# Optimization experiments

Hardware: AMD Instinct MI355X
Metric: run time of the kernel (lower is better)

The kernel has to match this reference:

```python
import jax, jax.numpy as jnp
import numpy as np

T, B, N_IN, H, N_OUT = 32, 32, 64, 256, 64
CLAMP_MIN, CLAMP_MAX = -2.0, 2.0  # scalar `min`/`max` forward args of the torch module


def setup_inputs() -> dict:
    key = jax.random.key(0)
    ks = jax.random.split(key, 8)
    s_ih = 1.0 / np.sqrt(N_IN)
    s_hh = 1.0 / np.sqrt(H)
    X = jax.random.normal(ks[0], (T, B, N_IN), jnp.float32)
    eps = jax.random.uniform(ks[1], (B,), jnp.float32) * 0.1  # per-sample perturbation radius
    W_ih = jax.random.normal(ks[2], (N_IN, H), jnp.float32) * s_ih  # already transposed, as in forward
    W_hh = jax.random.normal(ks[3], (H, H), jnp.float32) * s_hh
    b_ih = jax.random.normal(ks[4], (H,), jnp.float32) * s_hh
    b_hh = jax.random.normal(ks[5], (H,), jnp.float32) * s_hh
    W_o = jax.random.normal(ks[6], (H, N_OUT), jnp.float32) * s_hh
    b_o = jax.random.normal(ks[7], (N_OUT,), jnp.float32) * s_hh
    return dict(X=X, eps=eps, W_ih=W_ih, W_hh=W_hh, b_ih=b_ih, b_hh=b_hh, W_o=W_o, b_o=b_o)


def _zono_tanh(head, err):
    # DeepZ-style abstract tanh transformer on a zonotope (head [B,H], err [B,E,H]).
    rad = jnp.sum(jnp.abs(err), axis=1)                  # [B,H] concretization radius
    l, u = head - rad, head + rad
    tl, tu = jnp.tanh(l), jnp.tanh(u)
    lam = jnp.minimum(1.0 - tl * tl, 1.0 - tu * tu)      # minimal slope on [l,u]
    mu = 0.5 * (tu + tl - lam * (u + l))
    delta = 0.5 * (tu - tl - lam * (u - l))              # new error magnitude (>=0)
    new_head = lam * head + mu
    new_err = jnp.concatenate([lam[:, None, :] * err,
                               jax.vmap(jnp.diag)(delta)], axis=1)  # append H fresh symbols
    return new_head, new_err


def reference(X, eps, W_ih, W_hh, b_ih, b_hh, W_o, b_o):
    Bsz, Hn = X.shape[1], W_hh.shape[0]
    head_h = jnp.zeros((Bsz, Hn), X.dtype)
    err_h = jnp.zeros((Bsz, 0, Hn), X.dtype)
    bias = b_ih + b_hh
    for t in range(X.shape[0]):  # sequential recurrence; T is static
        x = X[t]                                          # [B, N_IN]
        l = jnp.maximum(x - eps[:, None], CLAMP_MIN)      # clamp(x-eps, min=min)
        u = jnp.minimum(x + eps[:, None], CLAMP_MAX)      # clamp(x+eps, max=max)
        head_x = 0.5 * (l + u)
        err_x = jax.vmap(jnp.diag)(0.5 * (u - l))         # diag_embed -> [B, N_IN, N_IN]
        # affine zonotope step: hx + hi + b_ih + b_hh
        head = head_x @ W_ih + head_h @ W_hh + bias       # [B, H]
        err = jnp.concatenate([err_h @ W_hh, err_x @ W_ih], axis=1)  # [B, E+N_IN, H]
        head_h, err_h = _zono_tanh(head, err)
    # output layer on the final zonotope; return concretized [lower, upper] bounds
    head_out = head_h @ W_o + b_o                         # [B, N_OUT]
    rad_out = jnp.sum(jnp.abs(err_h @ W_o), axis=1)       # [B, N_OUT]
    return jnp.stack([head_out - rad_out, head_out + rad_out])  # [2, B, N_OUT]
```

## Files before the change

### kernel.cpp

```cpp
#include <hip/hip_runtime.h>
#include <math.h>

typedef unsigned short u16;
typedef unsigned long long u64;
typedef __attribute__((ext_vector_type(8))) short bf16x8;
typedef __attribute__((ext_vector_type(4))) float f32x4;

#define T_STEPS 32
#define BSZ     32
#define N_IN    64
#define H       256
#define N_OUT   64
#define ESTRIDE 9984
#define CLAMP_MIN (-2.0f)
#define CLAMP_MAX ( 2.0f)
#define GNB 16


__device__ inline u16 f2bf(float x) {
    unsigned u = __builtin_bit_cast(unsigned, x);
    unsigned r = u + 0x7FFFu + ((u >> 16) & 1u);
    return (u16)(r >> 16);
}
__device__ inline float bf2f(short s) {
    return __builtin_bit_cast(float, ((unsigned)(u16)s) << 16);
}

__device__ __forceinline__ void gl_lds16(const u16* g, u16* l) {
    __builtin_amdgcn_global_load_lds(
        (const __attribute__((address_space(1))) unsigned int*)g,
        (__attribute__((address_space(3))) unsigned int*)l,
        16, 0, 0);
}

__global__ void transpose_k(const float* __restrict__ src, float* __restrict__ dst,
                            int R, int C)
{
    __shared__ float tile[32][33];
    int bi = blockIdx.y, bj = blockIdx.x;
    int r0 = threadIdx.x >> 5, c = threadIdx.x & 31;
    #pragma unroll
    for (int rr = 0; rr < 4; ++rr) {
        int r = r0 * 4 + rr;
        tile[r][c] = src[(bi * 32 + r) * C + bj * 32 + c];
    }
    __syncthreads();
    #pragma unroll
    for (int rr = 0; rr < 4; ++rr) {
        int r = r0 * 4 + rr;
        dst[(bj * 32 + r) * R + bi * 32 + c] = tile[c][r];
    }
}

__global__ void packPairs_k(const float* __restrict__ W, float* __restrict__ WP)
{
    int p = blockIdx.x * 256 + threadIdx.x;
    int vb = (p & 1) * 2, hh = (p >> 1) & 1, m = (p >> 2) & 15, qq = (p >> 6) & 3;
    int KC = (p >> 8) & 7, RT = p >> 11;
    int i = RT * 16 + m, k = KC * 32 + qq * 8 + hh * 4 + vb;
    ((float2*)WP)[p] = make_float2(W[(size_t)i * H + k], W[(size_t)i * H + k + 1]);
}

__global__ void packWT_k(const float* __restrict__ WT32, u16* __restrict__ WTp)
{
    int p = blockIdx.x * 256 + threadIdx.x;
    int vb = (p & 1) * 2, hh = (p >> 1) & 1, m = (p >> 2) & 15, qq = (p >> 6) & 3;
    int KC = (p >> 8) & 7, RT = p >> 11;
    int n = RT * 16 + m, k = KC * 32 + qq * 8 + hh * 4 + vb;
    *(unsigned*)&WTp[2 * p] =
          (unsigned)f2bf(WT32[(size_t)n * H + k])
        | ((unsigned)f2bf(WT32[(size_t)n * H + k + 1]) << 16);
}

__global__ __launch_bounds__(256) void prefresh_k(
    const float* __restrict__ X, const float* __restrict__ eps,
    const float* __restrict__ Wih, const float* __restrict__ WihP,
    const float* __restrict__ bih, const float* __restrict__ bhh,
    u16* __restrict__ err, float* __restrict__ radT, float* __restrict__ hp0)
{
    __shared__ float rho_s[N_IN], hx_s[N_IN];
    const int t = blockIdx.x, bi = blockIdx.y, tid = threadIdx.x;
    if (tid < N_IN) {
        float x = X[((size_t)t * BSZ + bi) * N_IN + tid], e = eps[bi];
        float lo = fmaxf(x - e, CLAMP_MIN), up = fminf(x + e, CLAMP_MAX);
        rho_s[tid] = 0.5f * (up - lo);
        hx_s[tid]  = 0.5f * (up + lo);
    }
    __syncthreads();

    float s = 0.f;
    #pragma unroll 8
    for (int i = 0; i < N_IN; ++i)
        s += fabsf(rho_s[i]) * fabsf(Wih[(size_t)i * H + tid]);
    radT[(size_t)t * BSZ * H + (size_t)bi * H + tid] = s;

    if (t == 0) {
        float acc = bih[tid] + bhh[tid];
        #pragma unroll 8
        for (int i = 0; i < N_IN; ++i) acc += hx_s[i] * Wih[i * H + tid];
        hp0[bi * H + tid] = acc;
    }

    u16* dst = err + (size_t)bi * ESTRIDE * H + (size_t)(20 * t) * 4096;
    const float2* wp = (const float2*)WihP;
    #pragma unroll 4
    for (int iter = 0; iter < 32; ++iter) {
        int p = iter * 256 + tid;
        int i = (p >> 11) * 16 + ((p >> 2) & 15);
        float2 w = wp[p];
        float rho = rho_s[i];
        *(unsigned*)&dst[2 * p] =
            (unsigned)f2bf(rho * w.x) | ((unsigned)f2bf(rho * w.y) << 16);
    }
}

__global__ __launch_bounds__(256, 2) void step_k(
    const float* __restrict__ Xt, const float* __restrict__ eps,
    const float* __restrict__ Wih, const float* __restrict__ Whh,
    const float* __restrict__ WhhP, const u16* __restrict__ WhhTp,
    const float* __restrict__ bih, const float* __restrict__ bhh,
    const float* __restrict__ hp_prev, const float* __restrict__ rad_prev,
    float* __restrict__ hp_new, float* __restrict__ rad_new,
    u16* __restrict__ err, int E_old)
{
    __shared__ u16 sbuf[4][8192];
    __shared__ float lam_s[H], de_s[H], hh_s[H], hx_s[N_IN];
    const int bx = blockIdx.x, b = blockIdx.y, tid = threadIdx.x;
    const int ntiles = (E_old - H) >> 5;
    u16* errB = err + (size_t)b * ESTRIDE * H;
    const int wave = tid >> 6, lane = tid & 63;
    const int m = lane & 15, q = lane >> 4;
    const bool gem = (bx < ntiles);

    if (gem) {
        #pragma unroll
        for (int j = 0; j < 3; ++j) {
            int tj = bx + j * GNB;
            if (tj < ntiles) {
                const u16* g = errB + (size_t)tj * 8192;
                #pragma unroll
                for (int r = 0; r < 4; ++r)
                    gl_lds16(g + r * 2048 + tid * 8, &sbuf[j][r * 2048 + wave * 512]);
            }
        }
    }

    bf16x8 bf[4][8];
    if (gem) {
        #pragma unroll
        for (int nt = 0; nt < 4; ++nt)
            #pragma unroll
            for (int kc = 0; kc < 8; ++kc)
                bf[nt][kc] = *(const bf16x8*)
                    &WhhTp[(size_t)(((((wave * 4 + nt) * 8 + kc) * 4 + q) << 7) + m * 8)];
    }

    {
        float hd = hp_prev[b * H + tid], rv = rad_prev[b * H + tid];
        float lo = hd - rv, up = hd + rv;
        float tl = tanhf(lo), tu = tanhf(up);
        float la = fminf(1.f - tl * tl, 1.f - tu * tu);
        float mu = 0.5f * (tu + tl - la * (up + lo));
        float dd = 0.5f * (tu - tl - la * (up - lo));
        lam_s[tid] = la;
        de_s[tid]  = dd;
        hh_s[tid]  = la * hd + mu;
    }
    asm volatile("s_waitcnt lgkmcnt(0)" ::: "memory");
    __builtin_amdgcn_s_barrier();

    if (gem) {
        #pragma unroll
        for (int nt = 0; nt < 4; ++nt)
            #pragma unroll
            for (int kc = 0; kc < 8; ++kc) {
                const int k0 = kc * 32 + q * 8;
                float4 la = *(const float4*)&lam_s[k0];
                float4 lb = *(const float4*)&lam_s[k0 + 4];
                bf16x8 w = bf[nt][kc], f;
                f[0] = (short)f2bf(bf2f(w[0]) * la.x);
                f[1] = (short)f2bf(bf2f(w[1]) * la.y);
                f[2] = (short)f2bf(bf2f(w[2]) * la.z);
                f[3] = (short)f2bf(bf2f(w[3]) * la.w);
                f[4] = (short)f2bf(bf2f(w[4]) * lb.x);
                f[5] = (short)f2bf(bf2f(w[5]) * lb.y);
                f[6] = (short)f2bf(bf2f(w[6]) * lb.z);
                f[7] = (short)f2bf(bf2f(w[7]) * lb.w);
                bf[nt][kc] = f;
            }

        float racc[16];
        #pragma unroll
        for (int i = 0; i < 16; ++i) racc[i] = 0.f;

        asm volatile("s_waitcnt vmcnt(0)" ::: "memory");
        __builtin_amdgcn_s_barrier();

        int cur = 0;
        for (int tile = bx; tile < ntiles; tile += GNB) {
            int pf = tile + 3 * GNB;
            if (pf < ntiles) {
                const u16* g = errB + (size_t)pf * 8192;
                #pragma unroll
                for (int r = 0; r < 4; ++r)
                    gl_lds16(g + r * 2048 + tid * 8,
                             &sbuf[(cur + 3) & 3][r * 2048 + wave * 512]);
            }

            f32x4 acc[2][4];
            #pragma unroll
            for (int i = 0; i < 2; ++i)
                #pragma unroll
                for (int c = 0; c < 4; ++c) acc[i][c] = (f32x4){0.f, 0.f, 0.f, 0.f};

            #pragma unroll
            for (int kc = 0; kc < 8; ++kc) {
                bf16x8 af[2];
                #pragma unroll
                for (int rt = 0; rt < 2; ++rt)
                    af[rt] = *(const bf16x8*)
                        &sbuf[cur][(((rt * 8 + kc) * 4 + q) << 7) + m * 8];
                #pragma unroll
                for (int nt = 0; nt < 4; ++nt)
                    #pragma unroll
                    for (int rt = 0; rt < 2; ++rt)
                        acc[rt][nt] = __builtin_amdgcn_mfma_f32_16x16x32_bf16(
                            bf[nt][kc], af[rt], acc[rt][nt], 0, 0, 0);
            }

            #pragma unroll
            for (int rt = 0; rt < 2; ++rt) {
                const size_t rowbase = (size_t)(tile * 2 + rt) * 4096;
                #pragma unroll
                for (int nt = 0; nt < 4; ++nt) {
                    f32x4 v = acc[rt][nt];
                    racc[nt * 4 + 0] += fabsf(v[0]);
                    racc[nt * 4 + 1] += fabsf(v[1]);
                    racc[nt * 4 + 2] += fabsf(v[2]);
                    racc[nt * 4 + 3] += fabsf(v[3]);
                    unsigned lo = (unsigned)f2bf(v[0]) | ((unsigned)f2bf(v[1]) << 16);
                    unsigned hi = (unsigned)f2bf(v[2]) | ((unsigned)f2bf(v[3]) << 16);
                    const int NT  = wave * 4 + nt;
                    const int kcs = NT >> 1;
                    const int qq  = (NT & 1) * 2 + (q >> 1);
                    const size_t off16 = rowbase
                        + (size_t)(((kcs * 4 + qq) << 7) + m * 8 + (q & 1) * 4);
                    *(u64*)&errB[off16] = ((u64)hi << 32) | lo;
                }
            }
            asm volatile("s_waitcnt vmcnt(32)" ::: "memory");
            __builtin_amdgcn_s_barrier();
            cur = (cur + 1) & 3;
        }

        #pragma unroll
        for (int i = 0; i < 16; ++i) {
            float v = racc[i];
            v += __shfl_xor(v, 1);
            v += __shfl_xor(v, 2);
            v += __shfl_xor(v, 4);
            v += __shfl_xor(v, 8);
            if (m == 0) {
                int nt = i >> 2, vv = i & 3;
                atomicAdd(&rad_new[b * H + wave * 64 + nt * 16 + q * 4 + vv], v);
            }
        }
    }

    const int diagRTbase = (E_old - H) >> 4;
    const float2* wp = (const float2*)WhhP;
    u16* dbase = errB + (size_t)(diagRTbase + bx) * 4096;
    #pragma unroll
    for (int iter = 0; iter < 8; ++iter) {
        int p = iter * 256 + tid;
        int mm = (p >> 2) & 15;
        float dv = de_s[bx * 16 + mm];
        float2 w = wp[bx * 2048 + p];
        *(unsigned*)&dbase[2 * p] =
            (unsigned)f2bf(dv * w.x) | ((unsigned)f2bf(dv * w.y) << 16);
    }
    float s = 0.f;
    #pragma unroll
    for (int ii = 0; ii < 16; ++ii) {
        int i = bx * 16 + ii;
        s += fabsf(de_s[i]) * fabsf(Whh[(size_t)i * H + tid]);
    }
    atomicAdd(&rad_new[b * H + tid], s);

    if (bx == GNB - 1) {
        if (tid < N_IN) {
            float x = Xt[b * N_IN + tid], e = eps[b];
            float l2 = fmaxf(x - e, CLAMP_MIN), u2 = fminf(x + e, CLAMP_MAX);
            hx_s[tid] = 0.5f * (l2 + u2);
        }
        __syncthreads();
        float acc = bih[tid] + bhh[tid];
        #pragma unroll 8
        for (int i = 0; i < N_IN; ++i) acc += hx_s[i] * Wih[i * H + tid];
        #pragma unroll 8
        for (int j = 0; j < H; ++j) acc += hh_s[j] * Whh[j * H + tid];
        hp_new[b * H + tid] = acc;
    }
}

__global__ __launch_bounds__(256) void tanh_final_k(
    const float* __restrict__ hp, const float* __restrict__ rad,
    float* __restrict__ lam, float* __restrict__ de, float* __restrict__ head_h)
{
    const int b = blockIdx.x, h = threadIdx.x;
    float hd = hp[b * H + h], r = rad[b * H + h];
    float l = hd - r, u = hd + r;
    float tl = tanhf(l), tu = tanhf(u);
    float la = fminf(1.f - tl * tl, 1.f - tu * tu);
    float mu = 0.5f * (tu + tl - la * (u + l));
    float dd = 0.5f * (tu - tl - la * (u - l));
    lam[b * H + h] = la;
    de[b * H + h]  = dd;
    head_h[b * H + h] = la * hd + mu;
}

__global__ __launch_bounds__(256) void packWoT_k(
    const float* __restrict__ WoT32, const float* __restrict__ lam,
    u16* __restrict__ WoTp)
{
    const int b = blockIdx.x, tid = threadIdx.x;
    __shared__ float lam_s[H];
    lam_s[tid] = lam[b * H + tid];
    __syncthreads();
    u16* dst = WoTp + (size_t)b * N_OUT * H;
    #pragma unroll 4
    for (int iter = 0; iter < 32; ++iter) {
        int p = iter * 256 + tid;
        int vb = (p & 1) * 2, hh = (p >> 1) & 1, m = (p >> 2) & 15, qq = (p >> 6) & 3;
        int KC = (p >> 8) & 7, RT = p >> 11;
        int n = RT * 16 + m, k = KC * 32 + qq * 8 + hh * 4 + vb;
        *(unsigned*)&dst[2 * p] =
              (unsigned)f2bf(lam_s[k]     * WoT32[(size_t)n * H + k])
            | ((unsigned)f2bf(lam_s[k + 1] * WoT32[(size_t)n * H + k + 1]) << 16);
    }
}

__global__ void head_out_k(
    const float* __restrict__ head_h, const float* __restrict__ de,
    const float* __restrict__ Wo, const float* __restrict__ bo,
    float* __restrict__ head_out, float* __restrict__ rad_out)
{
    const int b = blockIdx.x, o = threadIdx.x;
    float acc = bo[o], accR = 0.f;
    #pragma unroll 4
    for (int j = 0; j < H; ++j) {
        float w = Wo[j * N_OUT + o];
        acc  += head_h[b * H + j] * w;
        accR += fabsf(de[b * H + j] * w);
    }
    head_out[b * N_OUT + o] = acc;
    rad_out[b * N_OUT + o]  = accR;
}

__global__ __launch_bounds__(256) void gemm_out_k(
    const u16* __restrict__ err, const u16* __restrict__ WoTp,
    float* __restrict__ rad_out)
{
    __shared__ float rad_s[N_OUT];
    const int b = blockIdx.y, row0 = blockIdx.x * 256, tid = threadIdx.x;
    const int wave = tid >> 6, lane = tid & 63;
    const int m = lane & 15, q = lane >> 4;
    const u16* errB = err + (size_t)b * ESTRIDE * H;
    const u16* Wb   = WoTp + (size_t)b * N_OUT * H;

    if (tid < N_OUT) rad_s[tid] = 0.f;
    __syncthreads();

    f32x4 acc[4][4];
    #pragma unroll
    for (int i = 0; i < 4; ++i)
        #pragma unroll
        for (int c = 0; c < 4; ++c) acc[i][c] = (f32x4){0.f, 0.f, 0.f, 0.f};

    const int tile0 = (row0 >> 4) + wave * 4;
    #pragma unroll
    for (int kc = 0; kc < 8; ++kc) {
        bf16x8 af[4], bw[4];
        #pragma unroll
        for (int rt = 0; rt < 4; ++rt)
            af[rt] = *(const bf16x8*)
                &errB[(size_t)(((((tile0 + rt) * 8 + kc) * 4 + q) << 7) + m * 8)];
        #pragma unroll
        for (int nt = 0; nt < 4; ++nt)
            bw[nt] = *(const bf16x8*)
                &Wb[(size_t)((((nt * 8 + kc) * 4 + q) << 7) + m * 8)];
        #pragma unroll
        for (int nt = 0; nt < 4; ++nt)
            #pragma unroll
            for (int rt = 0; rt < 4; ++rt)
                acc[rt][nt] = __builtin_amdgcn_mfma_f32_16x16x32_bf16(
                    af[rt], bw[nt], acc[rt][nt], 0, 0, 0);
    }
    #pragma unroll
    for (int nt = 0; nt < 4; ++nt) {
        float s = 0.f;
        #pragma unroll
        for (int rt = 0; rt < 4; ++rt)
            #pragma unroll
            for (int r = 0; r < 4; ++r) s += fabsf(acc[rt][nt][r]);
        atomicAdd(&rad_s[nt * 16 + m], s);
    }
    __syncthreads();
    if (tid < N_OUT) atomicAdd(&rad_out[b * N_OUT + tid], rad_s[tid]);
}

__global__ void combine_k(const float* __restrict__ head_out,
                          const float* __restrict__ rad_out,
                          float* __restrict__ out)
{
    int i = blockIdx.x * 256 + threadIdx.x;
    if (i < BSZ * N_OUT) {
        float h = head_out[i], r = rad_out[i];
        out[i]               = h - r;
        out[BSZ * N_OUT + i] = h + r;
    }
}

extern "C" void kernel_launch(void* const* d_in, const int* in_sizes, int n_in,
                              void* d_out, int out_size, void* d_ws, size_t ws_size,
                              hipStream_t stream)
{
    const float* X    = (const float*)d_in[0];
    const float* eps  = (const float*)d_in[1];
    const float* Wih  = (const float*)d_in[2];
    const float* Whh  = (const float*)d_in[3];
    const float* bih  = (const float*)d_in[4];
    const float* bhh  = (const float*)d_in[5];
    const float* Wo   = (const float*)d_in[6];
    const float* bo   = (const float*)d_in[7];
    float* out = (float*)d_out;

    const size_t per_sample = (size_t)ESTRIDE * H * 2 + (size_t)N_OUT * H * 2;
    const size_t shared_b = (size_t)H * H * 4
                          + (size_t)N_OUT * H * 4
                          + (size_t)N_IN * H * 4
                          + (size_t)H * H * 4
                          + (size_t)H * H * 2
                          + (size_t)2 * BSZ * H * 4
                          + (size_t)T_STEPS * BSZ * H * 4
                          + (size_t)3 * BSZ * H * 4
                          + (size_t)2 * BSZ * N_OUT * 4 + 256;
    int Bc = BSZ;
    while (Bc > 1 && (size_t)Bc * per_sample + shared_b > ws_size) Bc >>= 1;

    char* p = (char*)d_ws;
    u16* errP      = (u16*)p;   p += (size_t)Bc * ESTRIDE * H * 2;
    u16* WoTp      = (u16*)p;   p += (size_t)Bc * N_OUT * H * 2;
    u16* WhhTp     = (u16*)p;   p += (size_t)H * H * 2;
    float* WhhT32  = (float*)p; p += (size_t)H * H * 4;
    float* WoT32   = (float*)p; p += (size_t)N_OUT * H * 4;
    float* WihP    = (float*)p; p += (size_t)N_IN * H * 4;
    float* WhhP    = (float*)p; p += (size_t)H * H * 4;
    float* hp      = (float*)p; p += (size_t)2 * BSZ * H * 4;
    float* radT    = (float*)p; p += (size_t)T_STEPS * BSZ * H * 4;
    float* lam     = (float*)p; p += (size_t)BSZ * H * 4;
    float* de      = (float*)p; p += (size_t)BSZ * H * 4;
    float* head_h  = (float*)p; p += (size_t)BSZ * H * 4;
    float* head_out= (float*)p; p += (size_t)BSZ * N_OUT * 4;
    float* rad_out = (float*)p;

    transpose_k<<<dim3(H / 32, H / 32), 256, 0, stream>>>(Whh, WhhT32, H, H);
    transpose_k<<<dim3(N_OUT / 32, H / 32), 256, 0, stream>>>(Wo, WoT32, H, N_OUT);
    packPairs_k<<<(N_IN * 128) / 256, 256, 0, stream>>>(Wih, WihP);
    packPairs_k<<<(H * 128) / 256, 256, 0, stream>>>(Whh, WhhP);
    packWT_k<<<128, 256, 0, stream>>>(WhhT32, WhhTp);

    for (int b0 = 0; b0 < BSZ; b0 += Bc) {
        prefresh_k<<<dim3(T_STEPS, Bc), 256, 0, stream>>>(
            X + (size_t)b0 * N_IN, eps + b0, Wih, WihP, bih, bhh, errP,
            radT + (size_t)b0 * H, hp + (size_t)b0 * H);
        for (int t = 1; t < T_STEPS; ++t) {
            int E_old = t * (N_IN + H);
            const float* hp_prev = hp + (size_t)((t - 1) & 1) * BSZ * H + (size_t)b0 * H;
            float*       hp_new  = hp + (size_t)(t & 1) * BSZ * H + (size_t)b0 * H;
            const float* rad_prev = radT + (size_t)(t - 1) * BSZ * H + (size_t)b0 * H;
            float*       rad_new  = radT + (size_t)t * BSZ * H + (size_t)b0 * H;
            step_k<<<dim3(GNB, Bc), 256, 0, stream>>>(
                X + (size_t)(t * BSZ + b0) * N_IN, eps + b0, Wih, Whh,
                WhhP, WhhTp, bih, bhh, hp_prev, rad_prev, hp_new, rad_new,
                errP, E_old);
        }
        const float* hp_last = hp + (size_t)((T_STEPS - 1) & 1) * BSZ * H + (size_t)b0 * H;
        const float* rad_last = radT + (size_t)(T_STEPS - 1) * BSZ * H + (size_t)b0 * H;
        tanh_final_k<<<Bc, 256, 0, stream>>>(
            hp_last, rad_last, lam + (size_t)b0 * H, de + (size_t)b0 * H,
            head_h + (size_t)b0 * H);
        packWoT_k<<<Bc, 256, 0, stream>>>(WoT32, lam + (size_t)b0 * H, WoTp);
        head_out_k<<<Bc, 64, 0, stream>>>(
            head_h + (size_t)b0 * H, de + (size_t)b0 * H, Wo, bo,
            head_out + (size_t)b0 * N_OUT, rad_out + (size_t)b0 * N_OUT);
        gemm_out_k<<<dim3(ESTRIDE / 256, Bc), 256, 0, stream>>>(
            errP, WoTp, rad_out + (size_t)b0 * N_OUT);
    }

    combine_k<<<(BSZ * N_OUT + 255) / 256, 256, 0, stream>>>(head_out, rad_out, out);
}
```

Before: 1.672 ms.

## Fuse recurrent step launches into one persistent kernel with grid barrier

Replaces the 31 per-timestep step_k launches with a single persistent loop_k kernel that iterates over timesteps and synchronizes all blocks through a global atomic barrier. The input-projection head for every timestep is now precomputed in prefresh_k, and the hidden-to-hidden head contribution is split across blocks with atomicAdd instead of being done serially by one block. This removes kernel launch gaps and the single-block tail per step. In exchange it depends on all 16×Bc blocks being co-resident for the spin barrier, and it relies on hpX and radT being correctly pre-initialised for the atomic accumulation.

```diff
diff --git a/kernel.cpp b/kernel.cpp
--- a/kernel.cpp
+++ b/kernel.cpp
@@ -33,6 +33,32 @@
         16, 0, 0);
 }
 
+__device__ __forceinline__ void gbar(unsigned* cnt, unsigned* gen) {
+    const unsigned nb = gridDim.x * gridDim.y;
+    __syncthreads();
+    if (threadIdx.x == 0) {
+        __threadfence();
+        unsigned g = __hip_atomic_load(gen, __ATOMIC_RELAXED,
+                                       __HIP_MEMORY_SCOPE_AGENT);
+        unsigned old = __hip_atomic_fetch_add(cnt, 1u, __ATOMIC_ACQ_REL,
+                                              __HIP_MEMORY_SCOPE_AGENT);
+        if (old == nb - 1u) {
+            __hip_atomic_store(cnt, 0u, __ATOMIC_RELAXED,
+                               __HIP_MEMORY_SCOPE_AGENT);
+            __hip_atomic_fetch_add(gen, 1u, __ATOMIC_RELEASE,
+                                   __HIP_MEMORY_SCOPE_AGENT);
+        } else {
+            while (__hip_atomic_load(gen, __ATOMIC_RELAXED,
+                                     __HIP_MEMORY_SCOPE_AGENT) == g)
+                __builtin_amdgcn_s_sleep(4);
+        }
+        __threadfence();
+    }
+    __syncthreads();
+}
+
+__global__ void initbar_k(unsigned* bar) { bar[0] = 0u; bar[1] = 0u; }
+
 __global__ void transpose_k(const float* __restrict__ src, float* __restrict__ dst,
                             int R, int C)
 {
@@ -76,7 +102,7 @@
     const float* __restrict__ X, const float* __restrict__ eps,
     const float* __restrict__ Wih, const float* __restrict__ WihP,
     const float* __restrict__ bih, const float* __restrict__ bhh,
-    u16* __restrict__ err, float* __restrict__ radT, float* __restrict__ hp0)
+    u16* __restrict__ err, float* __restrict__ radT, float* __restrict__ hpX)
 {
     __shared__ float rho_s[N_IN], hx_s[N_IN];
     const int t = blockIdx.x, bi = blockIdx.y, tid = threadIdx.x;
@@ -88,18 +114,15 @@
     }
     __syncthreads();
 
-    float s = 0.f;
+    float s = 0.f, acc = bih[tid] + bhh[tid];
     #pragma unroll 8
-    for (int i = 0; i < N_IN; ++i)
-        s += fabsf(rho_s[i]) * fabsf(Wih[(size_t)i * H + tid]);
+    for (int i = 0; i < N_IN; ++i) {
+        float w = Wih[(size_t)i * H + tid];
+        s   += fabsf(rho_s[i]) * fabsf(w);
+        acc += hx_s[i] * w;
+    }
     radT[(size_t)t * BSZ * H + (size_t)bi * H + tid] = s;
-
-    if (t == 0) {
-        float acc = bih[tid] + bhh[tid];
-        #pragma unroll 8
-        for (int i = 0; i < N_IN; ++i) acc += hx_s[i] * Wih[i * H + tid];
-        hp0[bi * H + tid] = acc;
-    }
+    hpX [(size_t)t * BSZ * H + (size_t)bi * H + tid] = acc;
 
     u16* dst = err + (size_t)bi * ESTRIDE * H + (size_t)(20 * t) * 4096;
     const float2* wp = (const float2*)WihP;
@@ -114,192 +137,190 @@
     }
 }
 
-__global__ __launch_bounds__(256, 2) void step_k(
-    const float* __restrict__ Xt, const float* __restrict__ eps,
-    const float* __restrict__ Wih, const float* __restrict__ Whh,
-    const float* __restrict__ WhhP, const u16* __restrict__ WhhTp,
-    const float* __restrict__ bih, const float* __restrict__ bhh,
-    const float* __restrict__ hp_prev, const float* __restrict__ rad_prev,
-    float* __restrict__ hp_new, float* __restrict__ rad_new,
-    u16* __restrict__ err, int E_old)
+__global__ __launch_bounds__(256, 2) void loop_k(
+    const float* __restrict__ Whh, const float* __restrict__ WhhP,
+    const u16* __restrict__ WhhTp,
+    float* __restrict__ hpX, float* __restrict__ radT,
+    u16* __restrict__ err, unsigned* __restrict__ bar, int b0)
 {
     __shared__ u16 sbuf[4][8192];
-    __shared__ float lam_s[H], de_s[H], hh_s[H], hx_s[N_IN];
+    __shared__ float lam_s[H], de_s[H], hh_s[H];
     const int bx = blockIdx.x, b = blockIdx.y, tid = threadIdx.x;
-    const int ntiles = (E_old - H) >> 5;
+    const int babs = b0 + b;
     u16* errB = err + (size_t)b * ESTRIDE * H;
     const int wave = tid >> 6, lane = tid & 63;
     const int m = lane & 15, q = lane >> 4;
-    const bool gem = (bx < ntiles);
-
-    if (gem) {
-        #pragma unroll
-        for (int j = 0; j < 3; ++j) {
-            int tj = bx + j * GNB;
-            if (tj < ntiles) {
-                const u16* g = errB + (size_t)tj * 8192;
+
+    for (int t = 1; t < T_STEPS; ++t) {
+        const int E_old = t * (N_IN + H);
+        const int ntiles = (E_old - H) >> 5;
+        const float* hpp  = hpX  + (size_t)(t - 1) * BSZ * H + (size_t)babs * H;
+        float*       hpn  = hpX  + (size_t)t       * BSZ * H + (size_t)babs * H;
+        const float* radp = radT + (size_t)(t - 1) * BSZ * H + (size_t)babs * H;
+        float*       radn = radT + (size_t)t       * BSZ * H + (size_t)babs * H;
+        const bool gem = (bx < ntiles);
+
+        if (gem) {
+            #pragma unroll
+            for (int j = 0; j < 3; ++j) {
+                int tj = bx + j * GNB;
+                if (tj < ntiles) {
+                    const u16* g = errB + (size_t)tj * 8192;
+                    #pragma unroll
+                    for (int r = 0; r < 4; ++r)
+                        gl_lds16(g + r * 2048 + tid * 8,
+                                 &sbuf[j][r * 2048 + wave * 512]);
+                }
+            }
+        }
+
+        bf16x8 bf[4][8];
+        if (gem) {
+            #pragma unroll
+            for (int nt = 0; nt < 4; ++nt)
                 #pragma unroll
-                for (int r = 0; r < 4; ++r)
-                    gl_lds16(g + r * 2048 + tid * 8, &sbuf[j][r * 2048 + wave * 512]);
-            }
-        }
-    }
-
-    bf16x8 bf[4][8];
-    if (gem) {
-        #pragma unroll
-        for (int nt = 0; nt < 4; ++nt)
-            #pragma unroll
-            for (int kc = 0; kc < 8; ++kc)
-                bf[nt][kc] = *(const bf16x8*)
-                    &WhhTp[(size_t)(((((wave * 4 + nt) * 8 + kc) * 4 + q) << 7) + m * 8)];
-    }
-
-    {
-        float hd = hp_prev[b * H + tid], rv = rad_prev[b * H + tid];
-        float lo = hd - rv, up = hd + rv;
-        float tl = tanhf(lo), tu = tanhf(up);
-        float la = fminf(1.f - tl * tl, 1.f - tu * tu);
-        float mu = 0.5f * (tu + tl - la * (up + lo));
-        float dd = 0.5f * (tu - tl - la * (up - lo));
-        lam_s[tid] = la;
-        de_s[tid]  = dd;
-        hh_s[tid]  = la * hd + mu;
-    }
-    asm volatile("s_waitcnt lgkmcnt(0)" ::: "memory");
-    __builtin_amdgcn_s_barrier();
-
-    if (gem) {
-        #pragma unroll
-        for (int nt = 0; nt < 4; ++nt)
-            #pragma unroll
-            for (int kc = 0; kc < 8; ++kc) {
-                const int k0 = kc * 32 + q * 8;
-                float4 la = *(const float4*)&lam_s[k0];
-                float4 lb = *(const float4*)&lam_s[k0 + 4];
-                bf16x8 w = bf[nt][kc], f;
-                f[0] = (short)f2bf(bf2f(w[0]) * la.x);
-                f[1] = (short)f2bf(bf2f(w[1]) * la.y);
-                f[2] = (short)f2bf(bf2f(w[2]) * la.z);
-                f[3] = (short)f2bf(bf2f(w[3]) * la.w);
-                f[4] = (short)f2bf(bf2f(w[4]) * lb.x);
-                f[5] = (short)f2bf(bf2f(w[5]) * lb.y);
-                f[6] = (short)f2bf(bf2f(w[6]) * lb.z);
-                f[7] = (short)f2bf(bf2f(w[7]) * lb.w);
-                bf[nt][kc] = f;
-            }
-
-        float racc[16];
-        #pragma unroll
-        for (int i = 0; i < 16; ++i) racc[i] = 0.f;
-
-        asm volatile("s_waitcnt vmcnt(0)" ::: "memory");
+                for (int kc = 0; kc < 8; ++kc)
+                    bf[nt][kc] = *(const bf16x8*)
+                        &WhhTp[(size_t)(((((wave * 4 + nt) * 8 + kc) * 4 + q) << 7) + m * 8)];
+        }
+
+        {
+            float hd = hpp[tid], rv = radp[tid];
+            float lo = hd - rv, up = hd + rv;
+            float tl = tanhf(lo), tu = tanhf(up);
+            float la = fminf(1.f - tl * tl, 1.f - tu * tu);
+            float mu = 0.5f * (tu + tl - la * (up + lo));
+            float dd = 0.5f * (tu - tl - la * (up - lo));
+            lam_s[tid] = la;
+            de_s[tid]  = dd;
+            hh_s[tid]  = la * hd + mu;
+        }
+        asm volatile("s_waitcnt lgkmcnt(0)" ::: "memory");
         __builtin_amdgcn_s_barrier();
 
-        int cur = 0;
-        for (int tile = bx; tile < ntiles; tile += GNB) {
-            int pf = tile + 3 * GNB;
-            if (pf < ntiles) {
-                const u16* g = errB + (size_t)pf * 8192;
+        if (gem) {
+            #pragma unroll
+            for (int nt = 0; nt < 4; ++nt)
                 #pragma unroll
-                for (int r = 0; r < 4; ++r)
-                    gl_lds16(g + r * 2048 + tid * 8,
-                             &sbuf[(cur + 3) & 3][r * 2048 + wave * 512]);
-            }
-
-            f32x4 acc[2][4];
-            #pragma unroll
-            for (int i = 0; i < 2; ++i)
+                for (int kc = 0; kc < 8; ++kc) {
+                    const int k0 = kc * 32 + q * 8;
+                    float4 la = *(const float4*)&lam_s[k0];
+                    float4 lb = *(const float4*)&lam_s[k0 + 4];
+                    bf16x8 w = bf[nt][kc], f;
+                    f[0] = (short)f2bf(bf2f(w[0]) * la.x);
+                    f[1] = (short)f2bf(bf2f(w[1]) * la.y);
+                    f[2] = (short)f2bf(bf2f(w[2]) * la.z);
+                    f[3] = (short)f2bf(bf2f(w[3]) * la.w);
+                    f[4] = (short)f2bf(bf2f(w[4]) * lb.x);
+                    f[5] = (short)f2bf(bf2f(w[5]) * lb.y);
+                    f[6] = (short)f2bf(bf2f(w[6]) * lb.z);
+                    f[7] = (short)f2bf(bf2f(w[7]) * lb.w);
+                    bf[nt][kc] = f;
+                }
+
+            float racc[16];
+            #pragma unroll
+            for (int i = 0; i < 16; ++i) racc[i] = 0.f;
+
+            asm volatile("s_waitcnt vmcnt(0)" ::: "memory");
+            __builtin_amdgcn_s_barrier();
+
+            int cur = 0;
+            for (int tile = bx; tile < ntiles; tile += GNB) {
+                int pf = tile + 3 * GNB;
+                if (pf < ntiles) {
+                    const u16* g = errB + (size_t)pf * 8192;
+                    #pragma unroll
+                    for (int r = 0; r < 4; ++r)
+                        gl_lds16(g + r * 2048 + tid * 8,
+                                 &sbuf[(cur + 3) & 3][r * 2048 + wave * 512]);
+                }
+
+                f32x4 acc[2][4];
                 #pragma unroll
-                for (int c = 0; c < 4; ++c) acc[i][c] = (f32x4){0.f, 0.f, 0.f, 0.f};
-
-            #pragma unroll
-            for (int kc = 0; kc < 8; ++kc) {
-                bf16x8 af[2];
+                for (int i = 0; i < 2; ++i)
+                    #pragma unroll
+                    for (int c = 0; c < 4; ++c) acc[i][c] = (f32x4){0.f, 0.f, 0.f, 0.f};
+
                 #pragma unroll
-                for (int rt = 0; rt < 2; ++rt)
-                    af[rt] = *(const bf16x8*)
-                        &sbuf[cur][(((rt * 8 + kc) * 4 + q) << 7) + m * 8];
-                #pragma unroll
-                for (int nt = 0; nt < 4; ++nt)
+                for (int kc = 0; kc < 8; ++kc) {
+                    bf16x8 af[2];
                     #pragma unroll
                     for (int rt = 0; rt < 2; ++rt)
-                        acc[rt][nt] = __builtin_amdgcn_mfma_f32_16x16x32_bf16(
-                            bf[nt][kc], af[rt], acc[rt][nt], 0, 0, 0);
+                        af[rt] = *(const bf16x8*)
+                            &sbuf[cur][(((rt * 8 + kc) * 4 + q) << 7) + m * 8];
+                    #pragma unroll
+                    for (int nt = 0; nt < 4; ++nt)
+                        #pragma unroll
+                        for (int rt = 0; rt < 2; ++rt)
+                            acc[rt][nt] = __builtin_amdgcn_mfma_f32_16x16x32_bf16(
+                                bf[nt][kc], af[rt], acc[rt][nt], 0, 0, 0);
+                }
+
+                #pragma unroll
+                for (int rt = 0; rt < 2; ++rt) {
+                    const size_t rowbase = (size_t)(tile * 2 + rt) * 4096;
+                    #pragma unroll
+                    for (int nt = 0; nt < 4; ++nt) {
+                        f32x4 v = acc[rt][nt];
+                        racc[nt * 4 + 0] += fabsf(v[0]);
+                        racc[nt * 4 + 1] += fabsf(v[1]);
+                        racc[nt * 4 + 2] += fabsf(v[2]);
+                        racc[nt * 4 + 3] += fabsf(v[3]);
+                        unsigned lo = (unsigned)f2bf(v[0]) | ((unsigned)f2bf(v[1]) << 16);
+                        unsigned hi = (unsigned)f2bf(v[2]) | ((unsigned)f2bf(v[3]) << 16);
+                        const int NT  = wave * 4 + nt;
+                        const int kcs = NT >> 1;
+                        const int qq  = (NT & 1) * 2 + (q >> 1);
+                        const size_t off16 = rowbase
+                            + (size_t)(((kcs * 4 + qq) << 7) + m * 8 + (q & 1) * 4);
+                        *(u64*)&errB[off16] = ((u64)hi << 32) | lo;
+                    }
+                }
+                asm volatile("s_waitcnt vmcnt(32)" ::: "memory");
+                __builtin_amdgcn_s_barrier();
+                cur = (cur + 1) & 3;
             }
 
             #pragma unroll
-            for (int rt = 0; rt < 2; ++rt) {
-                const size_t rowbase = (size_t)(tile * 2 + rt) * 4096;
-                #pragma unroll
-                for (int nt = 0; nt < 4; ++nt) {
-                    f32x4 v = acc[rt][nt];
-                    racc[nt * 4 + 0] += fabsf(v[0]);
-                    racc[nt * 4 + 1] += fabsf(v[1]);
-                    racc[nt * 4 + 2] += fabsf(v[2]);
-                    racc[nt * 4 + 3] += fabsf(v[3]);
-                    unsigned lo = (unsigned)f2bf(v[0]) | ((unsigned)f2bf(v[1]) << 16);
-                    unsigned hi = (unsigned)f2bf(v[2]) | ((unsigned)f2bf(v[3]) << 16);
-                    const int NT  = wave * 4 + nt;
-                    const int kcs = NT >> 1;
-                    const int qq  = (NT & 1) * 2 + (q >> 1);
-                    const size_t off16 = rowbase
-                        + (size_t)(((kcs * 4 + qq) << 7) + m * 8 + (q & 1) * 4);
-                    *(u64*)&errB[off16] = ((u64)hi << 32) | lo;
+            for (int i = 0; i < 16; ++i) {
+                float v = racc[i];
+                v += __shfl_xor(v, 1);
+                v += __shfl_xor(v, 2);
+                v += __shfl_xor(v, 4);
+                v += __shfl_xor(v, 8);
+                if (m == 0) {
+                    int nt = i >> 2, vv = i & 3;
+                    atomicAdd(&radn[wave * 64 + nt * 16 + q * 4 + vv], v);
                 }
             }
-            asm volatile("s_waitcnt vmcnt(32)" ::: "memory");
-            __builtin_amdgcn_s_barrier();
-            cur = (cur + 1) & 3;
-        }
-
-        #pragma unroll
-        for (int i = 0; i < 16; ++i) {
-            float v = racc[i];
-            v += __shfl_xor(v, 1);
-            v += __shfl_xor(v, 2);
-            v += __shfl_xor(v, 4);
-            v += __shfl_xor(v, 8);
-            if (m == 0) {
-                int nt = i >> 2, vv = i & 3;
-                atomicAdd(&rad_new[b * H + wave * 64 + nt * 16 + q * 4 + vv], v);
-            }
-        }
-    }
-
-    const int diagRTbase = (E_old - H) >> 4;
-    const float2* wp = (const float2*)WhhP;
-    u16* dbase = errB + (size_t)(diagRTbase + bx) * 4096;
-    #pragma unroll
-    for (int iter = 0; iter < 8; ++iter) {
-        int p = iter * 256 + tid;
-        int mm = (p >> 2) & 15;
-        float dv = de_s[bx * 16 + mm];
-        float2 w = wp[bx * 2048 + p];
-        *(unsigned*)&dbase[2 * p] =
-            (unsigned)f2bf(dv * w.x) | ((unsigned)f2bf(dv * w.y) << 16);
-    }
-    float s = 0.f;
-    #pragma unroll
-    for (int ii = 0; ii < 16; ++ii) {
-        int i = bx * 16 + ii;
-        s += fabsf(de_s[i]) * fabsf(Whh[(size_t)i * H + tid]);
-    }
-    atomicAdd(&rad_new[b * H + tid], s);
-
-    if (bx == GNB - 1) {
-        if (tid < N_IN) {
-            float x = Xt[b * N_IN + tid], e = eps[b];
-            float l2 = fmaxf(x - e, CLAMP_MIN), u2 = fminf(x + e, CLAMP_MAX);
-            hx_s[tid] = 0.5f * (l2 + u2);
-        }
-        __syncthreads();
-        float acc = bih[tid] + bhh[tid];
-        #pragma unroll 8
-        for (int i = 0; i < N_IN; ++i) acc += hx_s[i] * Wih[i * H + tid];
-        #pragma unroll 8
-        for (int j = 0; j < H; ++j) acc += hh_s[j] * Whh[j * H + tid];
-        hp_new[b * H + tid] = acc;
+        }
+
+        const int diagRTbase = (E_old - H) >> 4;
+        const float2* wp = (const float2*)WhhP;
+        u16* dbase = errB + (size_t)(diagRTbase + bx) * 4096;
+        #pragma unroll
+        for (int iter = 0; iter < 8; ++iter) {
+            int p = iter * 256 + tid;
+            int mm = (p >> 2) & 15;
+            float dv = de_s[bx * 16 + mm];
+            float2 w = wp[bx * 2048 + p];
+            *(unsigned*)&dbase[2 * p] =
+                (unsigned)f2bf(dv * w.x) | ((unsigned)f2bf(dv * w.y) << 16);
+        }
+        float s = 0.f, hacc = 0.f;
+        #pragma unroll
+        for (int ii = 0; ii < 16; ++ii) {
+            int i = bx * 16 + ii;
+            float w = Whh[(size_t)i * H + tid];
+            s    += fabsf(de_s[i]) * fabsf(w);
+            hacc += hh_s[i] * w;
+        }
+        atomicAdd(&radn[tid], s);
+        atomicAdd(&hpn[tid], hacc);
+
+        asm volatile("s_waitcnt vmcnt(0)" ::: "memory");
+        gbar(&bar[0], &bar[1]);
     }
 }
 
@@ -441,10 +462,10 @@
                           + (size_t)N_IN * H * 4
                           + (size_t)H * H * 4
                           + (size_t)H * H * 2
-                          + (size_t)2 * BSZ * H * 4
+                          + (size_t)T_STEPS * BSZ * H * 4
                           + (size_t)T_STEPS * BSZ * H * 4
                           + (size_t)3 * BSZ * H * 4
-                          + (size_t)2 * BSZ * N_OUT * 4 + 256;
+                          + (size_t)2 * BSZ * N_OUT * 4 + 512;
     int Bc = BSZ;
     while (Bc > 1 && (size_t)Bc * per_sample + shared_b > ws_size) Bc >>= 1;
 
@@ -456,14 +477,16 @@
     float* WoT32   = (float*)p; p += (size_t)N_OUT * H * 4;
     float* WihP    = (float*)p; p += (size_t)N_IN * H * 4;
     float* WhhP    = (float*)p; p += (size_t)H * H * 4;
-    float* hp      = (float*)p; p += (size_t)2 * BSZ * H * 4;
+    float* hpX     = (float*)p; p += (size_t)T_STEPS * BSZ * H * 4;
     float* radT    = (float*)p; p += (size_t)T_STEPS * BSZ * H * 4;
     float* lam     = (float*)p; p += (size_t)BSZ * H * 4;
     float* de      = (float*)p; p += (size_t)BSZ * H * 4;
     float* head_h  = (float*)p; p += (size_t)BSZ * H * 4;
     float* head_out= (float*)p; p += (size_t)BSZ * N_OUT * 4;
-    float* rad_out = (float*)p;
-
+    float* rad_out = (float*)p; p += (size_t)BSZ * N_OUT * 4 + 64;
+    unsigned* bar  = (unsigned*)p;
+
+    initbar_k<<<1, 1, 0, stream>>>(bar);
     transpose_k<<<dim3(H / 32, H / 32), 256, 0, stream>>>(Whh, WhhT32, H, H);
     transpose_k<<<dim3(N_OUT / 32, H / 32), 256, 0, stream>>>(Wo, WoT32, H, N_OUT);
     packPairs_k<<<(N_IN * 128) / 256, 256, 0, stream>>>(Wih, WihP);
@@ -473,19 +496,12 @@
     for (int b0 = 0; b0 < BSZ; b0 += Bc) {
         prefresh_k<<<dim3(T_STEPS, Bc), 256, 0, stream>>>(
             X + (size_t)b0 * N_IN, eps + b0, Wih, WihP, bih, bhh, errP,
-            radT + (size_t)b0 * H, hp + (size_t)b0 * H);
-        for (int t = 1; t < T_STEPS; ++t) {
-            int E_old = t * (N_IN + H);
-            const float* hp_prev = hp + (size_t)((t - 1) & 1) * BSZ * H + (size_t)b0 * H;
-            float*       hp_new  = hp + (size_t)(t & 1) * BSZ * H + (size_t)b0 * H;
-            const float* rad_prev = radT + (size_t)(t - 1) * BSZ * H + (size_t)b0 * H;
-            float*       rad_new  = radT + (size_t)t * BSZ * H + (size_t)b0 * H;
-            step_k<<<dim3(GNB, Bc), 256, 0, stream>>>(
-                X + (size_t)(t * BSZ + b0) * N_IN, eps + b0, Wih, Whh,
-                WhhP, WhhTp, bih, bhh, hp_prev, rad_prev, hp_new, rad_new,
-                errP, E_old);
-        }
-        const float* hp_last = hp + (size_t)((T_STEPS - 1) & 1) * BSZ * H + (size_t)b0 * H;
+            radT + (size_t)b0 * H, hpX + (size_t)b0 * H);
+
+        loop_k<<<dim3(GNB, Bc), 256, 0, stream>>>(
+            Whh, WhhP, WhhTp, hpX, radT, errP, bar, b0);
+
+        const float* hp_last  = hpX  + (size_t)(T_STEPS - 1) * BSZ * H + (size_t)b0 * H;
         const float* rad_last = radT + (size_t)(T_STEPS - 1) * BSZ * H + (size_t)b0 * H;
         tanh_final_k<<<Bc, 256, 0, stream>>>(
             hp_last, rad_last, lam + (size_t)b0 * H, de + (size_t)b0 * H,
```

Result: slower. 3.771 ms (+125.6%).
